# Performance work log

Measured on AMD Instinct MI355X. Metric: run time of the kernel, lower is better.

The kernel has to match this reference:

```python
import jax, jax.numpy as jnp
import numpy as np

SIGMA = 20.0  # outlier threshold used by FindOutliers
EPS = 1e-8


def setup_inputs() -> dict:
    key = jax.random.key(0)
    k1, k2, k3 = jax.random.split(key, 3)
    B, S, K, N = 2, 2048, 4096, 4096
    x = jax.random.normal(k1, (B, S, K), jnp.float32)
    # inject 8 outlier feature columns (|x| > sigma) so the fp correction path is exercised
    out_cols = jnp.arange(8) * (K // 8)
    x = x.at[:, :, out_cols].multiply(30.0)
    weight = jax.random.normal(k2, (N, K), jnp.float32) * (1.0 / np.sqrt(K))
    bias = jax.random.normal(k3, (N,), jnp.float32) * 0.01
    return {"x": x, "weight": weight, "bias": bias}


def reference(x, weight, bias):
    # x: [B,S,K], weight: [N,K], bias: [N]
    B, S, K = x.shape
    N = weight.shape[0]
    xf = x.reshape(-1, K)  # [M,K]

    # FindOutliers: columns where any activation exceeds sigma (as a fixed-size mask)
    col_mask = jnp.any(jnp.abs(xf) > SIGMA, axis=0)          # [K] bool
    keep = jnp.logical_not(col_mask)

    # weight quantization: zero outlier columns, per-output-row symmetric int8
    w_in = weight * keep[None, :].astype(weight.dtype)        # [N,K]
    q_scale = jnp.max(jnp.abs(w_in), axis=1) / 127.0          # [N]
    q_scale = jnp.maximum(q_scale, EPS)
    q_w = jnp.round(jnp.clip(w_in / q_scale[:, None], -128.0, 127.0)).astype(jnp.int8)

    # per-token (row) activation quantization (FindRowScaleF32)
    row_scale = jnp.max(jnp.abs(xf), axis=1, keepdims=True) / 127.0  # [M,1] fp32
    row_scale = jnp.maximum(row_scale, EPS)
    q_x = jnp.round(jnp.clip(xf / row_scale, -128.0, 127.0)).astype(jnp.int8)

    # int8 GEMM with int32 accumulation, then dequant + bias
    acc = jnp.matmul(q_x.astype(jnp.int32), q_w.T.astype(jnp.int32)).astype(jnp.float32)  # [M,N]
    y = acc * row_scale * q_scale[None, :]

    # fp outlier correction: x[:, ind] @ weight[:, ind].T  (dense masked form, same math)
    x_out = xf * col_mask[None, :].astype(xf.dtype)
    y = y + x_out @ weight.T

    y = y + bias[None, :]
    return y.reshape(B, S, N)
```

## Files before the change

### kernel.cpp

```cpp
#include <hip/hip_runtime.h>
#include <stdint.h>

#define K_DIM 4096
#define N_DIM 4096
#define SIGMA 20.0f
#define EPSQ 1e-8f

typedef __attribute__((ext_vector_type(4))) int i32x4;

#define GLDS16(gp, lp)                                                         \
  __builtin_amdgcn_global_load_lds(                                            \
      (const __attribute__((address_space(1))) unsigned int*)(const void*)(gp),\
      (__attribute__((address_space(3))) unsigned int*)(void*)(lp), 16, 0, 0)

__global__ __launch_bounds__(256) void k_rowquant(
    const float* __restrict__ x, float* __restrict__ row_scale,
    int* __restrict__ mask, int8_t* __restrict__ qx)
{
  const int m = blockIdx.x;
  const int t = threadIdx.x;
  const float4* xr = (const float4*)(x + (size_t)m * K_DIM);
  float4 v[4];
  float amax = 0.0f;
#pragma unroll
  for (int i = 0; i < 4; ++i) {
    v[i] = xr[t + i * 256];
    float a0 = fabsf(v[i].x), a1 = fabsf(v[i].y);
    float a2 = fabsf(v[i].z), a3 = fabsf(v[i].w);
    amax = fmaxf(amax, fmaxf(fmaxf(a0, a1), fmaxf(a2, a3)));
    int kbase = (t + i * 256) * 4;
    if (a0 > SIGMA) mask[kbase + 0] = 1;
    if (a1 > SIGMA) mask[kbase + 1] = 1;
    if (a2 > SIGMA) mask[kbase + 2] = 1;
    if (a3 > SIGMA) mask[kbase + 3] = 1;
  }
#pragma unroll
  for (int off = 32; off > 0; off >>= 1)
    amax = fmaxf(amax, __shfl_down(amax, off, 64));
  __shared__ float smax[4];
  __shared__ float sscale;
  if ((t & 63) == 0) smax[t >> 6] = amax;
  __syncthreads();
  if (t == 0) {
    float ms = fmaxf(fmaxf(smax[0], smax[1]), fmaxf(smax[2], smax[3]));
    float rs = fmaxf(ms / 127.0f, EPSQ);
    sscale = rs;
    row_scale[m] = rs;
  }
  __syncthreads();
  const float rs = sscale;
  uint32_t* qxo = (uint32_t*)(qx + (size_t)m * K_DIM);
#pragma unroll
  for (int i = 0; i < 4; ++i) {
    int q0 = (int)rintf(fminf(fmaxf(v[i].x / rs, -128.0f), 127.0f));
    int q1 = (int)rintf(fminf(fmaxf(v[i].y / rs, -128.0f), 127.0f));
    int q2 = (int)rintf(fminf(fmaxf(v[i].z / rs, -128.0f), 127.0f));
    int q3 = (int)rintf(fminf(fmaxf(v[i].w / rs, -128.0f), 127.0f));
    uint32_t packed = (uint32_t)(q0 & 0xff) | ((uint32_t)(q1 & 0xff) << 8) |
                      ((uint32_t)(q2 & 0xff) << 16) | ((uint32_t)(q3 & 0xff) << 24);
    qxo[t + i * 256] = packed;
  }
}

__global__ __launch_bounds__(256) void k_compact(
    const int* __restrict__ mask, int* __restrict__ outlist,
    int* __restrict__ count)
{
  int k = blockIdx.x * 256 + threadIdx.x;
  if (mask[k]) {
    int idx = atomicAdd(count, 1);
    outlist[idx] = k;
  }
}

__global__ __launch_bounds__(256) void k_wquant(
    const float* __restrict__ w, const int* __restrict__ mask,
    float* __restrict__ q_scale, int8_t* __restrict__ qw)
{
  const int n = blockIdx.x;
  const int t = threadIdx.x;
  const float4* wr = (const float4*)(w + (size_t)n * K_DIM);
  const int4* mr = (const int4*)mask;
  float4 v[4];
  float amax = 0.0f;
#pragma unroll
  for (int i = 0; i < 4; ++i) {
    float4 vv = wr[t + i * 256];
    int4 mm = mr[t + i * 256];
    vv.x = mm.x ? 0.0f : vv.x;
    vv.y = mm.y ? 0.0f : vv.y;
    vv.z = mm.z ? 0.0f : vv.z;
    vv.w = mm.w ? 0.0f : vv.w;
    v[i] = vv;
    amax = fmaxf(amax, fmaxf(fmaxf(fabsf(vv.x), fabsf(vv.y)),
                             fmaxf(fabsf(vv.z), fabsf(vv.w))));
  }
#pragma unroll
  for (int off = 32; off > 0; off >>= 1)
    amax = fmaxf(amax, __shfl_down(amax, off, 64));
  __shared__ float smax[4];
  __shared__ float sscale;
  if ((t & 63) == 0) smax[t >> 6] = amax;
  __syncthreads();
  if (t == 0) {
    float ms = fmaxf(fmaxf(smax[0], smax[1]), fmaxf(smax[2], smax[3]));
    float qs = fmaxf(ms / 127.0f, EPSQ);
    sscale = qs;
    q_scale[n] = qs;
  }
  __syncthreads();
  const float qs = sscale;
  uint32_t* qwo = (uint32_t*)(qw + (size_t)n * K_DIM);
#pragma unroll
  for (int i = 0; i < 4; ++i) {
    int q0 = (int)rintf(fminf(fmaxf(v[i].x / qs, -128.0f), 127.0f));
    int q1 = (int)rintf(fminf(fmaxf(v[i].y / qs, -128.0f), 127.0f));
    int q2 = (int)rintf(fminf(fmaxf(v[i].z / qs, -128.0f), 127.0f));
    int q3 = (int)rintf(fminf(fmaxf(v[i].w / qs, -128.0f), 127.0f));
    uint32_t packed = (uint32_t)(q0 & 0xff) | ((uint32_t)(q1 & 0xff) << 8) |
                      ((uint32_t)(q2 & 0xff) << 16) | ((uint32_t)(q3 & 0xff) << 24);
    qwo[t + i * 256] = packed;
  }
}

__global__ __launch_bounds__(512, 2) void k_gemm(
    const int8_t* __restrict__ qx, const int8_t* __restrict__ qw,
    const float* __restrict__ row_scale, const float* __restrict__ q_scale,
    const float* __restrict__ bias,
    const float* __restrict__ x, const float* __restrict__ w,
    const int* __restrict__ outlist, const int* __restrict__ outcount,
    float* __restrict__ out)
{
  __shared__ int8_t As[4][256 * 64];
  __shared__ int8_t Bs[4][256 * 64];

  const int t = threadIdx.x;
  const int m0 = blockIdx.y * 256;
  const int n0 = blockIdx.x * 256;
  const int lane = t & 63;
  const int wave = t >> 6;
  const int wm = (wave >> 2) * 128;
  const int wn = (wave & 3) * 64;
  const int lrow = lane & 15;
  const int kg = lane >> 4;

  i32x4 acc[8][4] = {};

  const int srow = t >> 2;
  const int sclog = (t & 3) ^ ((srow >> 1) & 3);
  const int8_t* gA = qx + (size_t)(m0 + srow) * K_DIM + sclog * 16;
  const int8_t* gB = qw + (size_t)(n0 + srow) * K_DIM + sclog * 16;

  int offA[8], offB[4];
#pragma unroll
  for (int i = 0; i < 8; ++i) {
    int rA = wm + i * 16 + lrow;
    offA[i] = rA * 64 + ((kg ^ ((rA >> 1) & 3)) * 16);
  }
#pragma unroll
  for (int j = 0; j < 4; ++j) {
    int rB = wn + j * 16 + lrow;
    offB[j] = rB * 64 + ((kg ^ ((rB >> 1) & 3)) * 16);
  }

#define STAGE_A(b, tt) do {                                                    \
    GLDS16(gA + (size_t)(tt) * 64, &As[b][t * 16]);                            \
    GLDS16(gA + (size_t)128 * K_DIM + (size_t)(tt) * 64, &As[b][8192 + t * 16]);\
  } while (0)
#define STAGE_B(b, tt) do {                                                    \
    GLDS16(gB + (size_t)(tt) * 64, &Bs[b][t * 16]);                            \
    GLDS16(gB + (size_t)128 * K_DIM + (size_t)(tt) * 64, &Bs[b][8192 + t * 16]);\
  } while (0)

  STAGE_A(0, 0); STAGE_B(0, 0);
  STAGE_A(1, 1); STAGE_B(1, 1);
  STAGE_A(2, 2); STAGE_B(2, 2);
  asm volatile("s_waitcnt vmcnt(8)" ::: "memory");
  __builtin_amdgcn_s_barrier();

#pragma unroll 4
  for (int kt = 0; kt < 64; ++kt) {
    const int cur = kt & 3;
    const int nx = (kt + 3) & 3;
    const int ktn = (kt + 3) & 63;
    const int8_t* a = &As[cur][0];
    const int8_t* b = &Bs[cur][0];

    i32x4 af[4], bf[4];
#pragma unroll
    for (int i = 0; i < 4; ++i) af[i] = *(const i32x4*)(a + offA[i]);
#pragma unroll
    for (int j = 0; j < 4; ++j) bf[j] = *(const i32x4*)(b + offB[j]);
    STAGE_A(nx, ktn);
    __builtin_amdgcn_s_barrier();
    asm volatile("s_waitcnt lgkmcnt(0)" ::: "memory");
    __builtin_amdgcn_sched_barrier(0);
    __builtin_amdgcn_s_setprio(1);
#pragma unroll
    for (int i = 0; i < 4; ++i)
#pragma unroll
      for (int j = 0; j < 4; ++j)
        acc[i][j] = __builtin_amdgcn_mfma_i32_16x16x64_i8(af[i], bf[j], acc[i][j], 0, 0, 0);
    __builtin_amdgcn_s_setprio(0);
    __builtin_amdgcn_s_barrier();

    i32x4 af2[4];
#pragma unroll
    for (int i = 0; i < 4; ++i) af2[i] = *(const i32x4*)(a + offA[4 + i]);
    STAGE_B(nx, ktn);
    __builtin_amdgcn_s_barrier();
    asm volatile("s_waitcnt lgkmcnt(0)" ::: "memory");
    __builtin_amdgcn_sched_barrier(0);
    __builtin_amdgcn_s_setprio(1);
#pragma unroll
    for (int i = 0; i < 4; ++i)
#pragma unroll
      for (int j = 0; j < 4; ++j)
        acc[4 + i][j] = __builtin_amdgcn_mfma_i32_16x16x64_i8(af2[i], bf[j], acc[4 + i][j], 0, 0, 0);
    __builtin_amdgcn_s_setprio(0);
    asm volatile("s_waitcnt vmcnt(8)" ::: "memory");
    __builtin_amdgcn_s_barrier();
  }

#undef STAGE_A
#undef STAGE_B

  __syncthreads();
  float* xsh = (float*)&As[0][0];
  float* wsh = (float*)&Bs[0][0];
  const int cnt = *outcount;
  const int cs = cnt < 8 ? cnt : 8;
#pragma unroll
  for (int u = 0; u < 4; ++u) {
    int idx = t * 4 + u;
    int rr = idx >> 3;
    int oo = idx & 7;
    float xv = 0.0f, wv = 0.0f;
    if (oo < cs) {
      int kcol = outlist[oo];
      xv = x[(size_t)(m0 + rr) * K_DIM + kcol];
      wv = w[(size_t)(n0 + rr) * K_DIM + kcol];
    }
    xsh[rr * 8 + oo] = xv;
    wsh[rr * 8 + oo] = wv;
  }
  __syncthreads();

  float qs[4], bv[4];
  int gn[4];
#pragma unroll
  for (int j = 0; j < 4; ++j) {
    gn[j] = n0 + wn + j * 16 + lrow;
    qs[j] = q_scale[gn[j]];
    bv[j] = bias[gn[j]];
  }

#pragma unroll
  for (int i = 0; i < 8; ++i) {
#pragma unroll
    for (int r = 0; r < 4; ++r) {
      int ml = wm + i * 16 + kg * 4 + r;
      int gm = m0 + ml;
      float rs = row_scale[gm];
      float xvv[8];
#pragma unroll
      for (int o = 0; o < 8; ++o) xvv[o] = xsh[ml * 8 + o];
#pragma unroll
      for (int j = 0; j < 4; ++j) {
        int nl = wn + j * 16 + lrow;
        float corr = 0.0f;
#pragma unroll
        for (int o = 0; o < 8; ++o) corr += xvv[o] * wsh[nl * 8 + o];
        for (int o = 8; o < cnt; ++o)
          corr += x[(size_t)gm * K_DIM + outlist[o]] *
                  w[(size_t)gn[j] * K_DIM + outlist[o]];
        float val = (float)acc[i][j][r] * rs * qs[j] + corr + bv[j];
        out[(size_t)gm * N_DIM + gn[j]] = val;
      }
    }
  }
}

extern "C" void kernel_launch(void* const* d_in, const int* in_sizes, int n_in,
                              void* d_out, int out_size, void* d_ws, size_t ws_size,
                              hipStream_t stream) {
  const float* x = (const float*)d_in[0];
  const float* w = (const float*)d_in[1];
  const float* bias = (const float*)d_in[2];
  float* out = (float*)d_out;
  const int M = in_sizes[0] / K_DIM;

  char* ws = (char*)d_ws;
  int* mask = (int*)(ws);
  int* count = (int*)(ws + 16384);
  int* outlist = (int*)(ws + 20480);
  float* row_scale = (float*)(ws + 36864);
  float* q_scale = (float*)(ws + 53248);
  int8_t* qx = (int8_t*)(ws + 131072);
  int8_t* qw = (int8_t*)(ws + 131072 + (size_t)M * K_DIM);

  hipMemsetAsync(ws, 0, 20480, stream);
  k_rowquant<<<M, 256, 0, stream>>>(x, row_scale, mask, qx);
  k_compact<<<K_DIM / 256, 256, 0, stream>>>(mask, outlist, count);
  k_wquant<<<N_DIM, 256, 0, stream>>>(w, mask, q_scale, qw);
  dim3 grid(N_DIM / 256, M / 256);
  k_gemm<<<grid, dim3(512, 1, 1), 0, stream>>>(qx, qw, row_scale, q_scale, bias,
                                               x, w, outlist, count, out);
}
```

Measured before the change: 248.1 us.

## Split GEMM k-step into four MFMA phases and replicate outlier mask

Result: slower. 259.0 us (+4.4%).

```diff
diff --git a/kernel.cpp b/kernel.cpp
--- a/kernel.cpp
+++ b/kernel.cpp
@@ -19,6 +19,7 @@
 {
   const int m = blockIdx.x;
   const int t = threadIdx.x;
+  int* mrep = mask + ((m & 7) << 12);
   const float4* xr = (const float4*)(x + (size_t)m * K_DIM);
   float4 v[4];
   float amax = 0.0f;
@@ -29,10 +30,10 @@
     float a2 = fabsf(v[i].z), a3 = fabsf(v[i].w);
     amax = fmaxf(amax, fmaxf(fmaxf(a0, a1), fmaxf(a2, a3)));
     int kbase = (t + i * 256) * 4;
-    if (a0 > SIGMA) mask[kbase + 0] = 1;
-    if (a1 > SIGMA) mask[kbase + 1] = 1;
-    if (a2 > SIGMA) mask[kbase + 2] = 1;
-    if (a3 > SIGMA) mask[kbase + 3] = 1;
+    if (a0 > SIGMA) mrep[kbase + 0] = 1;
+    if (a1 > SIGMA) mrep[kbase + 1] = 1;
+    if (a2 > SIGMA) mrep[kbase + 2] = 1;
+    if (a3 > SIGMA) mrep[kbase + 3] = 1;
   }
 #pragma unroll
   for (int off = 32; off > 0; off >>= 1)
@@ -62,12 +63,15 @@
   }
 }
 
-__global__ __launch_bounds__(256) void k_compact(
-    const int* __restrict__ mask, int* __restrict__ outlist,
-    int* __restrict__ count)
+__global__ __launch_bounds__(256) void k_collapse(
+    int* __restrict__ mask, int* __restrict__ outlist, int* __restrict__ count)
 {
   int k = blockIdx.x * 256 + threadIdx.x;
-  if (mask[k]) {
+  int v = 0;
+#pragma unroll
+  for (int r = 0; r < 8; ++r) v |= mask[(r << 12) + k];
+  mask[k] = v;
+  if (v) {
     int idx = atomicAdd(count, 1);
     outlist[idx] = k;
   }
@@ -163,18 +167,36 @@
     offB[j] = rB * 64 + ((kg ^ ((rB >> 1) & 3)) * 16);
   }
 
-#define STAGE_A(b, tt) do {                                                    \
-    GLDS16(gA + (size_t)(tt) * 64, &As[b][t * 16]);                            \
-    GLDS16(gA + (size_t)128 * K_DIM + (size_t)(tt) * 64, &As[b][8192 + t * 16]);\
+#define ST_A_LO(b, tt) GLDS16(gA + (size_t)(tt) * 64, &As[b][t * 16])
+#define ST_A_HI(b, tt) GLDS16(gA + (size_t)128 * K_DIM + (size_t)(tt) * 64, &As[b][8192 + t * 16])
+#define ST_B_LO(b, tt) GLDS16(gB + (size_t)(tt) * 64, &Bs[b][t * 16])
+#define ST_B_HI(b, tt) GLDS16(gB + (size_t)128 * K_DIM + (size_t)(tt) * 64, &Bs[b][8192 + t * 16])
+
+#define PHASE(aC, bC, IH, JH, STAGE_STMT) do {                                 \
+    i32x4 fa0 = *(const i32x4*)((aC) + offA[(IH) * 4 + 0]);                    \
+    i32x4 fa1 = *(const i32x4*)((aC) + offA[(IH) * 4 + 1]);                    \
+    i32x4 fa2 = *(const i32x4*)((aC) + offA[(IH) * 4 + 2]);                    \
+    i32x4 fa3 = *(const i32x4*)((aC) + offA[(IH) * 4 + 3]);                    \
+    i32x4 fb0 = *(const i32x4*)((bC) + offB[(JH) * 2 + 0]);                    \
+    i32x4 fb1 = *(const i32x4*)((bC) + offB[(JH) * 2 + 1]);                    \
+    STAGE_STMT;                                                                \
+    __builtin_amdgcn_s_barrier();                                              \
+    asm volatile("s_waitcnt lgkmcnt(0)" ::: "memory");                         \
+    __builtin_amdgcn_s_setprio(1);                                             \
+    acc[(IH)*4+0][(JH)*2+0] = __builtin_amdgcn_mfma_i32_16x16x64_i8(fa0, fb0, acc[(IH)*4+0][(JH)*2+0], 0, 0, 0); \
+    acc[(IH)*4+1][(JH)*2+0] = __builtin_amdgcn_mfma_i32_16x16x64_i8(fa1, fb0, acc[(IH)*4+1][(JH)*2+0], 0, 0, 0); \
+    acc[(IH)*4+2][(JH)*2+0] = __builtin_amdgcn_mfma_i32_16x16x64_i8(fa2, fb0, acc[(IH)*4+2][(JH)*2+0], 0, 0, 0); \
+    acc[(IH)*4+3][(JH)*2+0] = __builtin_amdgcn_mfma_i32_16x16x64_i8(fa3, fb0, acc[(IH)*4+3][(JH)*2+0], 0, 0, 0); \
+    acc[(IH)*4+0][(JH)*2+1] = __builtin_amdgcn_mfma_i32_16x16x64_i8(fa0, fb1, acc[(IH)*4+0][(JH)*2+1], 0, 0, 0); \
+    acc[(IH)*4+1][(JH)*2+1] = __builtin_amdgcn_mfma_i32_16x16x64_i8(fa1, fb1, acc[(IH)*4+1][(JH)*2+1], 0, 0, 0); \
+    acc[(IH)*4+2][(JH)*2+1] = __builtin_amdgcn_mfma_i32_16x16x64_i8(fa2, fb1, acc[(IH)*4+2][(JH)*2+1], 0, 0, 0); \
+    acc[(IH)*4+3][(JH)*2+1] = __builtin_amdgcn_mfma_i32_16x16x64_i8(fa3, fb1, acc[(IH)*4+3][(JH)*2+1], 0, 0, 0); \
+    __builtin_amdgcn_s_setprio(0);                                             \
   } while (0)
-#define STAGE_B(b, tt) do {                                                    \
-    GLDS16(gB + (size_t)(tt) * 64, &Bs[b][t * 16]);                            \
-    GLDS16(gB + (size_t)128 * K_DIM + (size_t)(tt) * 64, &Bs[b][8192 + t * 16]);\
-  } while (0)
-
-  STAGE_A(0, 0); STAGE_B(0, 0);
-  STAGE_A(1, 1); STAGE_B(1, 1);
-  STAGE_A(2, 2); STAGE_B(2, 2);
+
+  ST_A_LO(0, 0); ST_A_HI(0, 0); ST_B_LO(0, 0); ST_B_HI(0, 0);
+  ST_A_LO(1, 1); ST_A_HI(1, 1); ST_B_LO(1, 1); ST_B_HI(1, 1);
+  ST_A_LO(2, 2); ST_A_HI(2, 2); ST_B_LO(2, 2); ST_B_HI(2, 2);
   asm volatile("s_waitcnt vmcnt(8)" ::: "memory");
   __builtin_amdgcn_s_barrier();
 
@@ -186,44 +208,22 @@
     const int8_t* a = &As[cur][0];
     const int8_t* b = &Bs[cur][0];
 
-    i32x4 af[4], bf[4];
-#pragma unroll
-    for (int i = 0; i < 4; ++i) af[i] = *(const i32x4*)(a + offA[i]);
-#pragma unroll
-    for (int j = 0; j < 4; ++j) bf[j] = *(const i32x4*)(b + offB[j]);
-    STAGE_A(nx, ktn);
+    PHASE(a, b, 0, 0, ST_A_LO(nx, ktn));
     __builtin_amdgcn_s_barrier();
-    asm volatile("s_waitcnt lgkmcnt(0)" ::: "memory");
-    __builtin_amdgcn_sched_barrier(0);
-    __builtin_amdgcn_s_setprio(1);
-#pragma unroll
-    for (int i = 0; i < 4; ++i)
-#pragma unroll
-      for (int j = 0; j < 4; ++j)
-        acc[i][j] = __builtin_amdgcn_mfma_i32_16x16x64_i8(af[i], bf[j], acc[i][j], 0, 0, 0);
-    __builtin_amdgcn_s_setprio(0);
+    PHASE(a, b, 0, 1, ST_A_HI(nx, ktn));
     __builtin_amdgcn_s_barrier();
-
-    i32x4 af2[4];
-#pragma unroll
-    for (int i = 0; i < 4; ++i) af2[i] = *(const i32x4*)(a + offA[4 + i]);
-    STAGE_B(nx, ktn);
+    PHASE(a, b, 1, 0, ST_B_LO(nx, ktn));
     __builtin_amdgcn_s_barrier();
-    asm volatile("s_waitcnt lgkmcnt(0)" ::: "memory");
-    __builtin_amdgcn_sched_barrier(0);
-    __builtin_amdgcn_s_setprio(1);
-#pragma unroll
-    for (int i = 0; i < 4; ++i)
-#pragma unroll
-      for (int j = 0; j < 4; ++j)
-        acc[4 + i][j] = __builtin_amdgcn_mfma_i32_16x16x64_i8(af2[i], bf[j], acc[4 + i][j], 0, 0, 0);
-    __builtin_amdgcn_s_setprio(0);
+    PHASE(a, b, 1, 1, ST_B_HI(nx, ktn));
     asm volatile("s_waitcnt vmcnt(8)" ::: "memory");
     __builtin_amdgcn_s_barrier();
   }
 
-#undef STAGE_A
-#undef STAGE_B
+#undef PHASE
+#undef ST_A_LO
+#undef ST_A_HI
+#undef ST_B_LO
+#undef ST_B_HI
 
   __syncthreads();
   float* xsh = (float*)&As[0][0];
@@ -292,16 +292,16 @@
 
   char* ws = (char*)d_ws;
   int* mask = (int*)(ws);
-  int* count = (int*)(ws + 16384);
-  int* outlist = (int*)(ws + 20480);
-  float* row_scale = (float*)(ws + 36864);
-  float* q_scale = (float*)(ws + 53248);
-  int8_t* qx = (int8_t*)(ws + 131072);
-  int8_t* qw = (int8_t*)(ws + 131072 + (size_t)M * K_DIM);
-
-  hipMemsetAsync(ws, 0, 20480, stream);
+  int* count = (int*)(ws + 131072);
+  int* outlist = (int*)(ws + 135168);
+  float* row_scale = (float*)(ws + 151552);
+  float* q_scale = (float*)(ws + 167936);
+  int8_t* qx = (int8_t*)(ws + 262144);
+  int8_t* qw = (int8_t*)(ws + 262144 + (size_t)M * K_DIM);
+
+  hipMemsetAsync(ws, 0, 135680, stream);
   k_rowquant<<<M, 256, 0, stream>>>(x, row_scale, mask, qx);
-  k_compact<<<K_DIM / 256, 256, 0, stream>>>(mask, outlist, count);
+  k_collapse<<<K_DIM / 256, 256, 0, stream>>>(mask, outlist, count);
   k_wquant<<<N_DIM, 256, 0, stream>>>(w, mask, q_scale, qw);
   dim3 grid(N_DIM / 256, M / 256);
   k_gemm<<<grid, dim3(512, 1, 1), 0, stream>>>(qx, qw, row_scale, q_scale, bias,
```
